# Kernel optimization log

Hardware: AMD Instinct MI355X
Metric: run time of the kernel (lower is better)

The kernel has to match this reference:

```python
import jax, jax.numpy as jnp
import numpy as np
import math

T, B, I, H = 512, 64, 1024, 1024


def setup_inputs() -> dict:
    key = jax.random.key(0)
    k1, k2, k3, k4, k5 = jax.random.split(key, 5)
    stdv = 1.0 / math.sqrt(H)
    return {
        "input": jax.random.normal(k1, (T, B, I), dtype=jnp.float32),
        "h0": jnp.zeros((B, H), dtype=jnp.float32),
        "c0": jnp.zeros((B, H), dtype=jnp.float32),
        "W_x": jax.random.uniform(k2, (4 * H, I), minval=-stdv, maxval=stdv, dtype=jnp.float32),
        "W_h": jax.random.uniform(k3, (4 * H, H), minval=-stdv, maxval=stdv, dtype=jnp.float32),
        "b_x": jax.random.uniform(k4, (4 * H,), minval=-stdv, maxval=stdv, dtype=jnp.float32),
        "b_h": jax.random.uniform(k5, (4 * H,), minval=-stdv, maxval=stdv, dtype=jnp.float32),
    }


def reference(input, h0, c0, W_x, W_h, b_x, b_h):
    # weight_drop = 0.0 -> dropout is identity; W_h used as-is.
    # Precompute input projections for all timesteps in one big GEMM: [T,B,4H]
    gx_all = jnp.einsum("tbi,gi->tbg", input, W_x) + b_x + b_h

    hdim = W_h.shape[1]

    def step(carry, gx):
        h, c = carry
        g = gx + h @ W_h.T  # [B, 4H]
        xi, xf, xo, xn = jnp.split(g, 4, axis=1)
        i = jax.nn.sigmoid(xi)
        f = jax.nn.sigmoid(xf)
        o = jax.nn.sigmoid(xo)
        n = jnp.tanh(xn)
        c_new = f * c + i * n
        h_new = o * jnp.tanh(c_new)
        return (h_new, c_new), h_new

    (h_fin, c_fin), outputs = jax.lax.scan(step, (h0, c0), gx_all)
    return outputs, (h_fin, c_fin)
```

## Files before the change

### kernel.cpp

```cpp
#include <hip/hip_runtime.h>
#include <hip/hip_bf16.h>

#define T_STEPS 512
#define BATCH   64
#define IDIM    1024
#define HDIM    1024
#define GDIM    4096
#define UPB     16
#define LSTM_BLOCKS 64

typedef __attribute__((ext_vector_type(8))) short short8;
typedef __attribute__((ext_vector_type(8))) unsigned short ushort8;
typedef __attribute__((ext_vector_type(4))) float f32x4;

typedef __attribute__((address_space(1))) const unsigned int gas_uint;
typedef __attribute__((address_space(3))) unsigned int las_uint;

static __device__ __forceinline__ unsigned short f2bf(float f) {
    union { float f; unsigned u; } x; x.f = f;
    unsigned r = x.u + 0x7fffu + ((x.u >> 16) & 1u);
    return (unsigned short)(r >> 16);
}

static __device__ __forceinline__ short8 pack8(const float* p) {
    float4 v0 = *reinterpret_cast<const float4*>(p);
    float4 v1 = *reinterpret_cast<const float4*>(p + 4);
    short8 t;
    t[0]=(short)f2bf(v0.x); t[1]=(short)f2bf(v0.y);
    t[2]=(short)f2bf(v0.z); t[3]=(short)f2bf(v0.w);
    t[4]=(short)f2bf(v1.x); t[5]=(short)f2bf(v1.y);
    t[6]=(short)f2bf(v1.z); t[7]=(short)f2bf(v1.w);
    return t;
}

static __device__ __forceinline__ short8 ldg16(const unsigned short* p) {
    short8 d;
    asm volatile("global_load_dwordx4 %0, %1, off sc0 sc1" : "=v"(d) : "v"(p));
    return d;
}
static __device__ __forceinline__ void stg16(unsigned short* p, ushort8 v) {
    asm volatile("global_store_dwordx4 %0, %1, off sc0 sc1"
                 :: "v"(p), "v"(v) : "memory");
}

#define VMW(n) do { asm volatile("s_waitcnt vmcnt(" #n ")"); \
                    __builtin_amdgcn_sched_barrier(0); } while (0)

static __device__ __forceinline__ float fexp2(float x) {
    float r; asm("v_exp_f32 %0, %1" : "=v"(r) : "v"(x)); return r;
}
static __device__ __forceinline__ float frcp(float x) {
    float r; asm("v_rcp_f32 %0, %1" : "=v"(r) : "v"(x)); return r;
}
static __device__ __forceinline__ float fsigmoid(float x) {
    return frcp(1.f + fexp2(-1.4426950408889634f * x));
}
static __device__ __forceinline__ float ftanh(float x) {
    return 2.f * frcp(1.f + fexp2(-2.8853900817779268f * x)) - 1.f;
}

__global__ __launch_bounds__(256) void k_cast_bf16(
        const float* __restrict__ src, unsigned short* __restrict__ dst, int n8) {
    int stride = gridDim.x * 256;
    for (int i = blockIdx.x * 256 + threadIdx.x; i < n8; i += stride) {
        const float* p = src + (size_t)i * 8;
        float4 a = *reinterpret_cast<const float4*>(p);
        float4 b = *reinterpret_cast<const float4*>(p + 4);
        ushort8 v;
        v[0]=f2bf(a.x); v[1]=f2bf(a.y); v[2]=f2bf(a.z); v[3]=f2bf(a.w);
        v[4]=f2bf(b.x); v[5]=f2bf(b.y); v[6]=f2bf(b.z); v[7]=f2bf(b.w);
        *reinterpret_cast<ushort8*>(dst + (size_t)i * 8) = v;
    }
}

__global__ void k_h0_swz(const float* __restrict__ h0,
                         unsigned short* __restrict__ hbuf0) {
    int i = blockIdx.x * 256 + threadIdx.x;
    int m  = i >> 7;
    int hh = i & 127;
    const float* src = h0 + (size_t)m * HDIM + hh * 8;
    float4 a = *reinterpret_cast<const float4*>(src);
    float4 c = *reinterpret_cast<const float4*>(src + 4);
    ushort8 v;
    v[0]=f2bf(a.x); v[1]=f2bf(a.y); v[2]=f2bf(a.z); v[3]=f2bf(a.w);
    v[4]=f2bf(c.x); v[5]=f2bf(c.y); v[6]=f2bf(c.z); v[7]=f2bf(c.w);
    size_t dst16 = ((size_t)(m >> 4) * 32 + (hh >> 2)) * 64 + (m & 15) + 16 * (hh & 3);
    *reinterpret_cast<ushort8*>(hbuf0 + dst16 * 8) = v;
}

__global__ __launch_bounds__(256) void k_gx_gemm2(
        const unsigned short* __restrict__ Xb, const unsigned short* __restrict__ Wb,
        const float* __restrict__ bx, const float* __restrict__ bh,
        float* __restrict__ gx) {
    __shared__ __align__(16) unsigned short As[128 * 64];
    __shared__ __align__(16) unsigned short Bs[128 * 64];

    const int bid  = blockIdx.x;
    const int vbid = (bid & 7) * 1024 + (bid >> 3);
    const int nt   = vbid >> 8;
    const int mt   = vbid & 255;

    const int tid  = threadIdx.x;
    const int lane = tid & 63;
    const int w    = tid >> 6;
    const int l15  = lane & 15;
    const int wm   = (w >> 1) * 64;
    const int wn   = (w & 1) * 64;

    const int r8   = lane >> 3;
    const int csrc = (((lane & 7) ^ r8) << 4);

    const char* Xsrc[4]; const char* Wsrc[4];
#pragma unroll
    for (int i = 0; i < 4; ++i) {
        int row = w * 32 + i * 8 + r8;
        Xsrc[i] = (const char*)Xb + ((size_t)(mt * 128 + row) * IDIM) * 2 + csrc;
        Wsrc[i] = (const char*)Wb + ((size_t)(nt * 128 + row) * IDIM) * 2 + csrc;
    }

    f32x4 acc[4][4] = {};

    for (int k0 = 0; k0 < IDIM; k0 += 64) {
        __syncthreads();
#pragma unroll
        for (int i = 0; i < 4; ++i) {
            __builtin_amdgcn_global_load_lds(
                (gas_uint*)(Xsrc[i] + k0 * 2),
                (las_uint*)(As + (w * 32 + i * 8) * 64), 16, 0, 0);
            __builtin_amdgcn_global_load_lds(
                (gas_uint*)(Wsrc[i] + k0 * 2),
                (las_uint*)(Bs + (w * 32 + i * 8) * 64), 16, 0, 0);
        }
        asm volatile("s_waitcnt vmcnt(0)");
        __syncthreads();

        short8 af[2][4], bf_[2][4];
#pragma unroll
        for (int ks = 0; ks < 2; ++ks) {
            const int cl = ks * 64 + ((lane >> 4) << 4);
#pragma unroll
            for (int i = 0; i < 4; ++i) {
                const int ra = wm + i * 16 + l15;
                af[ks][i] = *reinterpret_cast<const short8*>(
                    (const char*)As + ra * 128 + (cl ^ ((ra & 7) << 4)));
                const int rb = wn + i * 16 + l15;
                bf_[ks][i] = *reinterpret_cast<const short8*>(
                    (const char*)Bs + rb * 128 + (cl ^ ((rb & 7) << 4)));
            }
        }
#pragma unroll
        for (int ks = 0; ks < 2; ++ks)
#pragma unroll
            for (int i = 0; i < 4; ++i)
#pragma unroll
                for (int j = 0; j < 4; ++j)
                    acc[i][j] = __builtin_amdgcn_mfma_f32_16x16x32_bf16(
                                    af[ks][i], bf_[ks][j], acc[i][j], 0, 0, 0);
    }

#pragma unroll
    for (int j = 0; j < 4; ++j) {
        int n = nt * 128 + wn + j * 16 + l15;
        float bb = bx[n] + bh[n];
#pragma unroll
        for (int i = 0; i < 4; ++i) {
            int mbase = mt * 128 + wm + i * 16 + (lane >> 4) * 4;
#pragma unroll
            for (int r = 0; r < 4; ++r)
                gx[(size_t)(mbase + r) * GDIM + n] = acc[i][j][r] + bb;
        }
    }
}

__global__ __launch_bounds__(256, 1) void k_lstm(
        const float* __restrict__ gx, const float* __restrict__ Wh,
        const float* __restrict__ cinit, float* __restrict__ out,
        unsigned short* __restrict__ hbuf, unsigned* __restrict__ bar) {
    __shared__ __align__(16) float gs[2][64][68];
    __shared__ __align__(16) unsigned short hs[64][16];

    const int b    = blockIdx.x;
    const int tid  = threadIdx.x;
    const int lane = tid & 63;
    const int w    = tid >> 6;
    const int rh   = w >> 1;
    const int kh   = w & 1;
    const int l15  = lane & 15;
    const int lk8  = (lane >> 4) * 8;

    short8 breg[64];
#pragma unroll
    for (int cg = 0; cg < 4; ++cg) {
        const float* wb = Wh + ((size_t)(cg * HDIM + b * UPB + l15)) * HDIM
                        + kh * 512 + lk8;
#pragma unroll
        for (int ks = 0; ks < 16; ++ks)
            breg[cg * 16 + ks] = pack8(wb + ks * 32);
    }

    const int m    = tid >> 2;
    const int q    = tid & 3;
    const int u0   = q * 4;
    const int col0 = b * UPB + u0;

    float4 c4 = *reinterpret_cast<const float4*>(&cinit[(size_t)m * HDIM + col0]);

    float4 gxv[4];
#pragma unroll
    for (int g = 0; g < 4; ++g)
        gxv[g] = *reinterpret_cast<const float4*>(
            &gx[(size_t)m * GDIM + g * HDIM + col0]);

    __syncthreads();

    const unsigned* fb = &bar[(kh * 32 + (lane & 31)) * 32];

    for (int t = 0; t < T_STEPS; ++t) {
        {
            unsigned v = __hip_atomic_load(fb, __ATOMIC_RELAXED,
                                           __HIP_MEMORY_SCOPE_AGENT);
            while (!__all((int)(v >= (unsigned)t))) {
                __builtin_amdgcn_s_sleep(2);
                v = __hip_atomic_load(fb, __ATOMIC_RELAXED,
                                      __HIP_MEMORY_SCOPE_AGENT);
            }
        }
        asm volatile("" ::: "memory");

        const unsigned short* hA2 = hbuf + (size_t)(t & 1) * (BATCH * HDIM)
                                  + ((size_t)rh * 64 + kh * 16) * 512 + lane * 8;
        short8 st[24];
#define SLOT(i) ((i) < 24 ? (i) : (i) - 24)
#define ISSK(ks) do { \
        st[SLOT((ks) * 2)]     = ldg16(hA2 + (ks) * 512);          \
        st[SLOT((ks) * 2 + 1)] = ldg16(hA2 + 16384 + (ks) * 512);  \
    } while (0)
#define CONS1(ks) do { \
        short8 a0 = st[SLOT((ks) * 2)], a1 = st[SLOT((ks) * 2 + 1)]; \
        accP0 = __builtin_amdgcn_mfma_f32_16x16x32_bf16(a0, breg[(ks)],      accP0, 0, 0, 0); \
        accP1 = __builtin_amdgcn_mfma_f32_16x16x32_bf16(a0, breg[16 + (ks)], accP1, 0, 0, 0); \
        accP2 = __builtin_amdgcn_mfma_f32_16x16x32_bf16(a0, breg[32 + (ks)], accP2, 0, 0, 0); \
        accP3 = __builtin_amdgcn_mfma_f32_16x16x32_bf16(a0, breg[48 + (ks)], accP3, 0, 0, 0); \
        accQ0 = __builtin_amdgcn_mfma_f32_16x16x32_bf16(a1, breg[(ks)],      accQ0, 0, 0, 0); \
        accQ1 = __builtin_amdgcn_mfma_f32_16x16x32_bf16(a1, breg[16 + (ks)], accQ1, 0, 0, 0); \
        accQ2 = __builtin_amdgcn_mfma_f32_16x16x32_bf16(a1, breg[32 + (ks)], accQ2, 0, 0, 0); \
        accQ3 = __builtin_amdgcn_mfma_f32_16x16x32_bf16(a1, breg[48 + (ks)], accQ3, 0, 0, 0); \
    } while (0)

        f32x4 accP0 = {}, accP1 = {}, accP2 = {}, accP3 = {};
        f32x4 accQ0 = {}, accQ1 = {}, accQ2 = {}, accQ3 = {};
        ISSK(0); ISSK(1); ISSK(2);  ISSK(3);  ISSK(4);  ISSK(5);
        ISSK(6); ISSK(7); ISSK(8);  ISSK(9);  ISSK(10); ISSK(11);
        VMW(16); CONS1(0);  CONS1(1);  CONS1(2);  CONS1(3);
        ISSK(12); ISSK(13); ISSK(14); ISSK(15);
        VMW(16); CONS1(4);  CONS1(5);  CONS1(6);  CONS1(7);
        VMW(8);  CONS1(8);  CONS1(9);  CONS1(10); CONS1(11);
        VMW(0);  CONS1(12); CONS1(13); CONS1(14); CONS1(15);
#undef SLOT
#undef ISSK
#undef CONS1

        {
            const int gr = rh * 32 + (lane >> 4) * 4;
#pragma unroll
            for (int r = 0; r < 4; ++r) {
                gs[kh][gr + r][l15]           = accP0[r];
                gs[kh][gr + r][16 + l15]      = accP1[r];
                gs[kh][gr + r][32 + l15]      = accP2[r];
                gs[kh][gr + r][48 + l15]      = accP3[r];
                gs[kh][gr + 16 + r][l15]      = accQ0[r];
                gs[kh][gr + 16 + r][16 + l15] = accQ1[r];
                gs[kh][gr + 16 + r][32 + l15] = accQ2[r];
                gs[kh][gr + 16 + r][48 + l15] = accQ3[r];
            }
        }
        __syncthreads();

        float4 hv4;
        {
            float4 s0[4], s1[4];
#pragma unroll
            for (int g = 0; g < 4; ++g) {
                s0[g] = *reinterpret_cast<const float4*>(&gs[0][m][g * 16 + u0]);
                s1[g] = *reinterpret_cast<const float4*>(&gs[1][m][g * 16 + u0]);
            }
#pragma unroll
            for (int j = 0; j < 4; ++j) {
                float xi = gxv[0][j] + s0[0][j] + s1[0][j];
                float xf = gxv[1][j] + s0[1][j] + s1[1][j];
                float xo = gxv[2][j] + s0[2][j] + s1[2][j];
                float xn = gxv[3][j] + s0[3][j] + s1[3][j];
                float ig = fsigmoid(xi);
                float fg = fsigmoid(xf);
                float og = fsigmoid(xo);
                float ng = ftanh(xn);
                c4[j] = fg * c4[j] + ig * ng;
                hv4[j] = og * ftanh(c4[j]);
            }
            unsigned p0 = (unsigned)f2bf(hv4.x) | ((unsigned)f2bf(hv4.y) << 16);
            unsigned p1 = (unsigned)f2bf(hv4.z) | ((unsigned)f2bf(hv4.w) << 16);
            uint2 pk; pk.x = p0; pk.y = p1;
            *reinterpret_cast<uint2*>(&hs[m][u0]) = pk;
        }

        if (t == T_STEPS - 1) {
            size_t fin = (size_t)T_STEPS * BATCH * HDIM;
            *reinterpret_cast<float4*>(
                &out[((size_t)t * BATCH + m) * HDIM + col0]) = hv4;
            *reinterpret_cast<float4*>(
                &out[fin + (size_t)m * HDIM + col0]) = hv4;
            *reinterpret_cast<float4*>(
                &out[fin + (size_t)BATCH * HDIM + (size_t)m * HDIM + col0]) = c4;
            break;
        }

        __syncthreads();

        if (tid < 128) {
            const int mm = tid >> 1;
            const int hh = tid & 1;
            ushort8 v = *reinterpret_cast<const ushort8*>(&hs[mm][hh * 8]);
            size_t dst16 = ((size_t)(mm >> 4) * 32 + (b >> 1)) * 64 + (mm & 15)
                         + 16 * (((b & 1) << 1) | hh);
            stg16(hbuf + (size_t)((t + 1) & 1) * (BATCH * HDIM) + dst16 * 8, v);
        }
        __syncthreads();
        if (tid == 0)
            __hip_atomic_store(&bar[b * 32], (unsigned)(t + 1),
                               __ATOMIC_RELAXED, __HIP_MEMORY_SCOPE_AGENT);

        *reinterpret_cast<float4*>(
            &out[((size_t)t * BATCH + m) * HDIM + col0]) = hv4;
        {
            const float* gp = gx + (size_t)(t + 1) * BATCH * GDIM
                            + (size_t)m * GDIM + col0;
#pragma unroll
            for (int g = 0; g < 4; ++g)
                gxv[g] = *reinterpret_cast<const float4*>(gp + g * HDIM);
        }
        VMW(0);
    }
}

extern "C" void kernel_launch(void* const* d_in, const int* in_sizes, int n_in,
                              void* d_out, int out_size, void* d_ws, size_t ws_size,
                              hipStream_t stream) {
    const float* X  = (const float*)d_in[0];
    const float* h0 = (const float*)d_in[1];
    const float* c0 = (const float*)d_in[2];
    const float* Wx = (const float*)d_in[3];
    const float* Wh = (const float*)d_in[4];
    const float* bx = (const float*)d_in[5];
    const float* bh = (const float*)d_in[6];
    float* out = (float*)d_out;

    char* ws = (char*)d_ws;
    float* gx = (float*)ws;
    size_t gx_bytes = (size_t)T_STEPS * BATCH * GDIM * 4;
    unsigned short* hbuf = (unsigned short*)(ws + gx_bytes);
    size_t hbuf_bytes = (size_t)2 * BATCH * HDIM * 2;
    unsigned* bar = (unsigned*)(ws + gx_bytes + hbuf_bytes);

    unsigned short* Xb  = (unsigned short*)d_out;
    unsigned short* Wxb = Xb + (size_t)T_STEPS * BATCH * IDIM;

    hipMemsetAsync(bar, 0, LSTM_BLOCKS * 32 * sizeof(unsigned), stream);
    k_cast_bf16<<<dim3(2048), dim3(256), 0, stream>>>(
        X, Xb, (int)((size_t)T_STEPS * BATCH * IDIM / 8));
    k_cast_bf16<<<dim3(512), dim3(256), 0, stream>>>(
        Wx, Wxb, (int)((size_t)GDIM * IDIM / 8));
    k_h0_swz<<<dim3(32), dim3(256), 0, stream>>>(h0, hbuf);
    k_gx_gemm2<<<dim3(8192), dim3(256), 0, stream>>>(Xb, Wxb, bx, bh, gx);
    k_lstm<<<dim3(LSTM_BLOCKS), dim3(256), 0, stream>>>(gx, Wh, c0, out, hbuf, bar);
}
```

Before: 2.501 ms.

## Fuse input-projection GEMM with persistent LSTM recurrence via per-tile readiness flags

```diff
diff --git a/kernel.cpp b/kernel.cpp
--- a/kernel.cpp
+++ b/kernel.cpp
@@ -7,14 +7,13 @@
 #define HDIM    1024
 #define GDIM    4096
 #define UPB     16
-#define LSTM_BLOCKS 64
+#define NGEMM   192
+#define NREC    64
+#define NTILES  8192
 
 typedef __attribute__((ext_vector_type(8))) short short8;
 typedef __attribute__((ext_vector_type(8))) unsigned short ushort8;
 typedef __attribute__((ext_vector_type(4))) float f32x4;
-
-typedef __attribute__((address_space(1))) const unsigned int gas_uint;
-typedef __attribute__((address_space(3))) unsigned int las_uint;
 
 static __device__ __forceinline__ unsigned short f2bf(float f) {
     union { float f; unsigned u; } x; x.f = f;
@@ -38,10 +37,28 @@
     asm volatile("global_load_dwordx4 %0, %1, off sc0 sc1" : "=v"(d) : "v"(p));
     return d;
 }
+static __device__ __forceinline__ f32x4 ldg16f(const float* p) {
+    f32x4 d;
+    asm volatile("global_load_dwordx4 %0, %1, off sc0 sc1" : "=v"(d) : "v"(p));
+    return d;
+}
 static __device__ __forceinline__ void stg16(unsigned short* p, ushort8 v) {
     asm volatile("global_store_dwordx4 %0, %1, off sc0 sc1"
                  :: "v"(p), "v"(v) : "memory");
 }
+static __device__ __forceinline__ void stgf(float* p, float v) {
+    asm volatile("global_store_dword %0, %1, off sc0 sc1"
+                 :: "v"(p), "v"(v) : "memory");
+}
+static __device__ __forceinline__ unsigned ldflag(const unsigned* p) {
+    unsigned d;
+    asm volatile("global_load_dword %0, %1, off sc0 sc1" : "=v"(d) : "v"(p));
+    return d;
+}
+static __device__ __forceinline__ void stflag(unsigned* p, unsigned v) {
+    asm volatile("global_store_dword %0, %1, off sc0 sc1"
+                 :: "v"(p), "v"(v) : "memory");
+}
 
 #define VMW(n) do { asm volatile("s_waitcnt vmcnt(" #n ")"); \
                     __builtin_amdgcn_sched_barrier(0); } while (0)
@@ -57,20 +74,6 @@
 }
 static __device__ __forceinline__ float ftanh(float x) {
     return 2.f * frcp(1.f + fexp2(-2.8853900817779268f * x)) - 1.f;
-}
-
-__global__ __launch_bounds__(256) void k_cast_bf16(
-        const float* __restrict__ src, unsigned short* __restrict__ dst, int n8) {
-    int stride = gridDim.x * 256;
-    for (int i = blockIdx.x * 256 + threadIdx.x; i < n8; i += stride) {
-        const float* p = src + (size_t)i * 8;
-        float4 a = *reinterpret_cast<const float4*>(p);
-        float4 b = *reinterpret_cast<const float4*>(p + 4);
-        ushort8 v;
-        v[0]=f2bf(a.x); v[1]=f2bf(a.y); v[2]=f2bf(a.z); v[3]=f2bf(a.w);
-        v[4]=f2bf(b.x); v[5]=f2bf(b.y); v[6]=f2bf(b.z); v[7]=f2bf(b.w);
-        *reinterpret_cast<ushort8*>(dst + (size_t)i * 8) = v;
-    }
 }
 
 __global__ void k_h0_swz(const float* __restrict__ h0,
@@ -88,110 +91,113 @@
     *reinterpret_cast<ushort8*>(hbuf0 + dst16 * 8) = v;
 }
 
-__global__ __launch_bounds__(256) void k_gx_gemm2(
-        const unsigned short* __restrict__ Xb, const unsigned short* __restrict__ Wb,
+__global__ __launch_bounds__(256, 1) void k_fused(
+        const float* __restrict__ X, const float* __restrict__ Wx,
         const float* __restrict__ bx, const float* __restrict__ bh,
-        float* __restrict__ gx) {
+        const float* __restrict__ Wh, const float* __restrict__ cinit,
+        float* __restrict__ out, float* __restrict__ gx,
+        unsigned short* __restrict__ hbuf, unsigned* __restrict__ bar,
+        unsigned* __restrict__ cnt, unsigned* __restrict__ mtdone) {
     __shared__ __align__(16) unsigned short As[128 * 64];
     __shared__ __align__(16) unsigned short Bs[128 * 64];
+    __shared__ __align__(16) float gs[2][64][68];
+    __shared__ __align__(16) unsigned short hs[64][16];
 
     const int bid  = blockIdx.x;
-    const int vbid = (bid & 7) * 1024 + (bid >> 3);
-    const int nt   = vbid >> 8;
-    const int mt   = vbid & 255;
-
     const int tid  = threadIdx.x;
     const int lane = tid & 63;
     const int w    = tid >> 6;
     const int l15  = lane & 15;
-    const int wm   = (w >> 1) * 64;
-    const int wn   = (w & 1) * 64;
-
-    const int r8   = lane >> 3;
-    const int csrc = (((lane & 7) ^ r8) << 4);
-
-    const char* Xsrc[4]; const char* Wsrc[4];
-#pragma unroll
-    for (int i = 0; i < 4; ++i) {
-        int row = w * 32 + i * 8 + r8;
-        Xsrc[i] = (const char*)Xb + ((size_t)(mt * 128 + row) * IDIM) * 2 + csrc;
-        Wsrc[i] = (const char*)Wb + ((size_t)(nt * 128 + row) * IDIM) * 2 + csrc;
+
+    if (bid < NGEMM) {
+        const int wm   = (w >> 1) * 64;
+        const int wn   = (w & 1) * 64;
+        const int arow = tid >> 1;
+        const int ch   = tid & 1;
+        const int rsw  = (arow & 7) << 4;
+        const int nt   = bid & 31;
+        char* Adst = (char*)As + arow * 128;
+        char* Bdst = (char*)Bs + arow * 128;
+
+        for (int tau = bid; tau < NTILES; tau += NGEMM) {
+            const int mt = tau >> 5;
+            const float* Abase = X  + (size_t)(mt * 128 + arow) * IDIM + ch * 32;
+            const float* Bbase = Wx + (size_t)(nt * 128 + arow) * IDIM + ch * 32;
+            f32x4 acc[4][4] = {};
+
+            for (int k0 = 0; k0 < IDIM; k0 += 64) {
+                short8 av[4], bv[4];
+#pragma unroll
+                for (int q = 0; q < 4; ++q) {
+                    av[q] = pack8(Abase + k0 + q * 8);
+                    bv[q] = pack8(Bbase + k0 + q * 8);
+                }
+                __syncthreads();
+#pragma unroll
+                for (int q = 0; q < 4; ++q) {
+                    const int cb = ch * 64 + q * 16;
+                    *reinterpret_cast<short8*>(Adst + (cb ^ rsw)) = av[q];
+                    *reinterpret_cast<short8*>(Bdst + (cb ^ rsw)) = bv[q];
+                }
+                __syncthreads();
+
+                short8 af[2][4], bf_[2][4];
+#pragma unroll
+                for (int ks = 0; ks < 2; ++ks) {
+                    const int cl = ks * 64 + ((lane >> 4) << 4);
+#pragma unroll
+                    for (int i = 0; i < 4; ++i) {
+                        const int ra = wm + i * 16 + l15;
+                        af[ks][i] = *reinterpret_cast<const short8*>(
+                            (const char*)As + ra * 128 + (cl ^ ((ra & 7) << 4)));
+                        const int rb2 = wn + i * 16 + l15;
+                        bf_[ks][i] = *reinterpret_cast<const short8*>(
+                            (const char*)Bs + rb2 * 128 + (cl ^ ((rb2 & 7) << 4)));
+                    }
+                }
+#pragma unroll
+                for (int ks = 0; ks < 2; ++ks)
+#pragma unroll
+                    for (int i = 0; i < 4; ++i)
+#pragma unroll
+                        for (int j = 0; j < 4; ++j)
+                            acc[i][j] = __builtin_amdgcn_mfma_f32_16x16x32_bf16(
+                                af[ks][i], bf_[ks][j], acc[i][j], 0, 0, 0);
+            }
+
+#pragma unroll
+            for (int j = 0; j < 4; ++j) {
+                int n = nt * 128 + wn + j * 16 + l15;
+                float bb = bx[n] + bh[n];
+#pragma unroll
+                for (int i = 0; i < 4; ++i) {
+                    int mbase = mt * 128 + wm + i * 16 + (lane >> 4) * 4;
+#pragma unroll
+                    for (int r = 0; r < 4; ++r)
+                        stgf(&gx[(size_t)(mbase + r) * GDIM + n],
+                             acc[i][j][r] + bb);
+                }
+            }
+            VMW(0);
+            __syncthreads();
+            if (tid == 0) {
+                unsigned old = __hip_atomic_fetch_add(&cnt[mt], 1u,
+                                   __ATOMIC_RELAXED, __HIP_MEMORY_SCOPE_AGENT);
+                if (old == 31u) stflag(&mtdone[mt * 32], 1u);
+            }
+        }
+        return;
     }
 
-    f32x4 acc[4][4] = {};
-
-    for (int k0 = 0; k0 < IDIM; k0 += 64) {
-        __syncthreads();
-#pragma unroll
-        for (int i = 0; i < 4; ++i) {
-            __builtin_amdgcn_global_load_lds(
-                (gas_uint*)(Xsrc[i] + k0 * 2),
-                (las_uint*)(As + (w * 32 + i * 8) * 64), 16, 0, 0);
-            __builtin_amdgcn_global_load_lds(
-                (gas_uint*)(Wsrc[i] + k0 * 2),
-                (las_uint*)(Bs + (w * 32 + i * 8) * 64), 16, 0, 0);
-        }
-        asm volatile("s_waitcnt vmcnt(0)");
-        __syncthreads();
-
-        short8 af[2][4], bf_[2][4];
-#pragma unroll
-        for (int ks = 0; ks < 2; ++ks) {
-            const int cl = ks * 64 + ((lane >> 4) << 4);
-#pragma unroll
-            for (int i = 0; i < 4; ++i) {
-                const int ra = wm + i * 16 + l15;
-                af[ks][i] = *reinterpret_cast<const short8*>(
-                    (const char*)As + ra * 128 + (cl ^ ((ra & 7) << 4)));
-                const int rb = wn + i * 16 + l15;
-                bf_[ks][i] = *reinterpret_cast<const short8*>(
-                    (const char*)Bs + rb * 128 + (cl ^ ((rb & 7) << 4)));
-            }
-        }
-#pragma unroll
-        for (int ks = 0; ks < 2; ++ks)
-#pragma unroll
-            for (int i = 0; i < 4; ++i)
-#pragma unroll
-                for (int j = 0; j < 4; ++j)
-                    acc[i][j] = __builtin_amdgcn_mfma_f32_16x16x32_bf16(
-                                    af[ks][i], bf_[ks][j], acc[i][j], 0, 0, 0);
-    }
-
-#pragma unroll
-    for (int j = 0; j < 4; ++j) {
-        int n = nt * 128 + wn + j * 16 + l15;
-        float bb = bx[n] + bh[n];
-#pragma unroll
-        for (int i = 0; i < 4; ++i) {
-            int mbase = mt * 128 + wm + i * 16 + (lane >> 4) * 4;
-#pragma unroll
-            for (int r = 0; r < 4; ++r)
-                gx[(size_t)(mbase + r) * GDIM + n] = acc[i][j][r] + bb;
-        }
-    }
-}
-
-__global__ __launch_bounds__(256, 1) void k_lstm(
-        const float* __restrict__ gx, const float* __restrict__ Wh,
-        const float* __restrict__ cinit, float* __restrict__ out,
-        unsigned short* __restrict__ hbuf, unsigned* __restrict__ bar) {
-    __shared__ __align__(16) float gs[2][64][68];
-    __shared__ __align__(16) unsigned short hs[64][16];
-
-    const int b    = blockIdx.x;
-    const int tid  = threadIdx.x;
-    const int lane = tid & 63;
-    const int w    = tid >> 6;
-    const int rh   = w >> 1;
-    const int kh   = w & 1;
-    const int l15  = lane & 15;
-    const int lk8  = (lane >> 4) * 8;
+    const int rb  = bid - NGEMM;
+    const int rh  = w >> 1;
+    const int kh  = w & 1;
+    const int lk8 = (lane >> 4) * 8;
 
     short8 breg[64];
 #pragma unroll
     for (int cg = 0; cg < 4; ++cg) {
-        const float* wb = Wh + ((size_t)(cg * HDIM + b * UPB + l15)) * HDIM
+        const float* wb = Wh + ((size_t)(cg * HDIM + rb * UPB + l15)) * HDIM
                         + kh * 512 + lk8;
 #pragma unroll
         for (int ks = 0; ks < 16; ++ks)
@@ -201,15 +207,21 @@
     const int m    = tid >> 2;
     const int q    = tid & 3;
     const int u0   = q * 4;
-    const int col0 = b * UPB + u0;
-
-    float4 c4 = *reinterpret_cast<const float4*>(&cinit[(size_t)m * HDIM + col0]);
-
-    float4 gxv[4];
+    const int col0 = rb * UPB + u0;
+
+    f32x4 c4 = *reinterpret_cast<const f32x4*>(&cinit[(size_t)m * HDIM + col0]);
+
+    {
+        unsigned d = ldflag(&mtdone[0]); VMW(0);
+        while (!d) {
+            __builtin_amdgcn_s_sleep(8);
+            d = ldflag(&mtdone[0]); VMW(0);
+        }
+    }
+    f32x4 gxv[4];
 #pragma unroll
     for (int g = 0; g < 4; ++g)
-        gxv[g] = *reinterpret_cast<const float4*>(
-            &gx[(size_t)m * GDIM + g * HDIM + col0]);
+        gxv[g] = ldg16f(&gx[(size_t)m * GDIM + g * HDIM + col0]);
 
     __syncthreads();
 
@@ -217,12 +229,14 @@
 
     for (int t = 0; t < T_STEPS; ++t) {
         {
-            unsigned v = __hip_atomic_load(fb, __ATOMIC_RELAXED,
-                                           __HIP_MEMORY_SCOPE_AGENT);
-            while (!__all((int)(v >= (unsigned)t))) {
+            int need = (t + 1) >> 1; if (need > 255) need = 255;
+            const unsigned* mdp = &mtdone[need * 32];
+            while (true) {
+                unsigned v = ldflag(fb);
+                unsigned d = ldflag(mdp);
+                VMW(0);
+                if (__all(((int)(v >= (unsigned)t)) & (int)(d != 0))) break;
                 __builtin_amdgcn_s_sleep(2);
-                v = __hip_atomic_load(fb, __ATOMIC_RELAXED,
-                                      __HIP_MEMORY_SCOPE_AGENT);
             }
         }
         asm volatile("" ::: "memory");
@@ -276,13 +290,13 @@
         }
         __syncthreads();
 
-        float4 hv4;
+        f32x4 hv4;
         {
-            float4 s0[4], s1[4];
+            f32x4 s0[4], s1[4];
 #pragma unroll
             for (int g = 0; g < 4; ++g) {
-                s0[g] = *reinterpret_cast<const float4*>(&gs[0][m][g * 16 + u0]);
-                s1[g] = *reinterpret_cast<const float4*>(&gs[1][m][g * 16 + u0]);
+                s0[g] = *reinterpret_cast<const f32x4*>(&gs[0][m][g * 16 + u0]);
+                s1[g] = *reinterpret_cast<const f32x4*>(&gs[1][m][g * 16 + u0]);
             }
 #pragma unroll
             for (int j = 0; j < 4; ++j) {
@@ -297,19 +311,19 @@
                 c4[j] = fg * c4[j] + ig * ng;
                 hv4[j] = og * ftanh(c4[j]);
             }
-            unsigned p0 = (unsigned)f2bf(hv4.x) | ((unsigned)f2bf(hv4.y) << 16);
-            unsigned p1 = (unsigned)f2bf(hv4.z) | ((unsigned)f2bf(hv4.w) << 16);
+            unsigned p0 = (unsigned)f2bf(hv4[0]) | ((unsigned)f2bf(hv4[1]) << 16);
+            unsigned p1 = (unsigned)f2bf(hv4[2]) | ((unsigned)f2bf(hv4[3]) << 16);
             uint2 pk; pk.x = p0; pk.y = p1;
             *reinterpret_cast<uint2*>(&hs[m][u0]) = pk;
         }
 
         if (t == T_STEPS - 1) {
             size_t fin = (size_t)T_STEPS * BATCH * HDIM;
-            *reinterpret_cast<float4*>(
+            *reinterpret_cast<f32x4*>(
                 &out[((size_t)t * BATCH + m) * HDIM + col0]) = hv4;
-            *reinterpret_cast<float4*>(
+            *reinterpret_cast<f32x4*>(
                 &out[fin + (size_t)m * HDIM + col0]) = hv4;
-            *reinterpret_cast<float4*>(
+            *reinterpret_cast<f32x4*>(
                 &out[fin + (size_t)BATCH * HDIM + (size_t)m * HDIM + col0]) = c4;
             break;
         }
@@ -320,23 +334,23 @@
             const int mm = tid >> 1;
             const int hh = tid & 1;
             ushort8 v = *reinterpret_cast<const ushort8*>(&hs[mm][hh * 8]);
-            size_t dst16 = ((size_t)(mm >> 4) * 32 + (b >> 1)) * 64 + (mm & 15)
-                         + 16 * (((b & 1) << 1) | hh);
+            size_t dst16 = ((size_t)(mm >> 4) * 32 + (rb >> 1)) * 64 + (mm & 15)
+                         + 16 * (((rb & 1) << 1) | hh);
             stg16(hbuf + (size_t)((t + 1) & 1) * (BATCH * HDIM) + dst16 * 8, v);
         }
         __syncthreads();
         if (tid == 0)
-            __hip_atomic_store(&bar[b * 32], (unsigned)(t + 1),
+            __hip_atomic_store(&bar[rb * 32], (unsigned)(t + 1),
                                __ATOMIC_RELAXED, __HIP_MEMORY_SCOPE_AGENT);
 
-        *reinterpret_cast<float4*>(
+        *reinterpret_cast<f32x4*>(
             &out[((size_t)t * BATCH + m) * HDIM + col0]) = hv4;
         {
             const float* gp = gx + (size_t)(t + 1) * BATCH * GDIM
                             + (size_t)m * GDIM + col0;
 #pragma unroll
             for (int g = 0; g < 4; ++g)
-                gxv[g] = *reinterpret_cast<const float4*>(gp + g * HDIM);
+                gxv[g] = ldg16f(gp + g * HDIM);
         }
         VMW(0);
     }
@@ -359,17 +373,13 @@
     size_t gx_bytes = (size_t)T_STEPS * BATCH * GDIM * 4;
     unsigned short* hbuf = (unsigned short*)(ws + gx_bytes);
     size_t hbuf_bytes = (size_t)2 * BATCH * HDIM * 2;
-    unsigned* bar = (unsigned*)(ws + gx_bytes + hbuf_bytes);
-
-    unsigned short* Xb  = (unsigned short*)d_out;
-    unsigned short* Wxb = Xb + (size_t)T_STEPS * BATCH * IDIM;
-
-    hipMemsetAsync(bar, 0, LSTM_BLOCKS * 32 * sizeof(unsigned), stream);
-    k_cast_bf16<<<dim3(2048), dim3(256), 0, stream>>>(
-        X, Xb, (int)((size_t)T_STEPS * BATCH * IDIM / 8));
-    k_cast_bf16<<<dim3(512), dim3(256), 0, stream>>>(
-        Wx, Wxb, (int)((size_t)GDIM * IDIM / 8));
+    char* sync_base = ws + gx_bytes + hbuf_bytes;
+    unsigned* bar    = (unsigned*)sync_base;
+    unsigned* cnt    = (unsigned*)(sync_base + 8192);
+    unsigned* mtdone = (unsigned*)(sync_base + 12288);
+
+    hipMemsetAsync(sync_base, 0, 45056, stream);
     k_h0_swz<<<dim3(32), dim3(256), 0, stream>>>(h0, hbuf);
-    k_gx_gemm2<<<dim3(8192), dim3(256), 0, stream>>>(Xb, Wxb, bx, bh, gx);
-    k_lstm<<<dim3(LSTM_BLOCKS), dim3(256), 0, stream>>>(gx, Wh, c0, out, hbuf, bar);
-}
+    k_fused<<<dim3(NGEMM + NREC), dim3(256), 0, stream>>>(
+        X, Wx, bx, bh, Wh, c0, out, gx, hbuf, bar, cnt, mtdone);
+}
```

Result: faster. 2.222 ms, median of 2 (-11.2%).
